# Kernel optimization log

Measured on AMD Instinct MI355X. Metric: run time of the kernel, lower is better.

## Reference

```python
import jax, jax.numpy as jnp
import numpy as np

LAYERS = 2
N_NODE = 100000
EMB = 112
BATCH = 512
SEQ = 50
NNZ = 1600000


def setup_inputs() -> dict:
    key = jax.random.key(0)
    ks = jax.random.split(key, 12)
    embedding = jax.random.normal(ks[0], (N_NODE, EMB), jnp.float32) * 0.1
    adj_rows = jax.random.randint(ks[1], (NNZ,), 0, N_NODE, jnp.int32)
    adj_cols = jax.random.randint(ks[2], (NNZ,), 0, N_NODE, jnp.int32)
    adj_vals = jax.random.uniform(ks[3], (NNZ,), jnp.float32) * 0.05  # normalized-ish weights
    W_q = jax.random.normal(ks[4], (EMB, EMB), jnp.float32) * 0.1
    W_k = jax.random.normal(ks[5], (EMB, EMB), jnp.float32) * 0.1
    w_sess = jax.random.normal(ks[6], (LAYERS, EMB, EMB), jnp.float32) * 0.1
    D = jax.random.uniform(ks[7], (BATCH, BATCH), jnp.float32) * 0.01
    A = jax.random.uniform(ks[8], (BATCH, BATCH), jnp.float32)
    session_len = jax.random.randint(ks[9], (BATCH, 1), 1, SEQ + 1, jnp.int32)
    mask = (jnp.arange(SEQ)[None, :] < session_len).astype(jnp.float32)  # [B,L]
    raw_items = jax.random.randint(ks[10], (BATCH, SEQ), 1, N_NODE + 1, jnp.int32)
    session_item = jnp.where(mask > 0, raw_items, 0)  # 0 = padding row in cl_embed
    return {
        "embedding": embedding, "adj_vals": adj_vals, "W_q": W_q, "W_k": W_k,
        "w_sess": w_sess, "D": D, "A": A, "adj_rows": adj_rows,
        "adj_cols": adj_cols, "session_item": session_item,
        "session_len": session_len, "mask": mask,
    }


def reference(embedding, adj_vals, W_q, W_k, w_sess, D, A,
              adj_rows, adj_cols, session_item, session_len, mask):
    dt = embedding.dtype
    # ---- HyperConv: layers x sparse.mm, then mean over layer stack ----
    emb = embedding
    acc = embedding
    for _ in range(LAYERS):
        msg = adj_vals[:, None] * emb[adj_cols]              # [nnz, d]
        emb = jax.ops.segment_sum(msg, adj_rows, num_segments=N_NODE)
        acc = acc + emb
    item_emb = acc / (LAYERS + 1)                            # [N, d]

    # ---- SR_IEM sigmoid attention pooling ----
    d = jnp.asarray(EMB, dt)
    cl = jnp.concatenate([jnp.zeros((1, EMB), dt), item_emb], axis=0)
    seq = cl[session_item]                                   # [B,L,d]
    Q = jax.nn.sigmoid(jnp.einsum('bld,de->ble', seq, W_q))
    K = jax.nn.sigmoid(jnp.einsum('bld,de->ble', seq, W_k))
    C = jax.nn.sigmoid(jnp.einsum('ble,bme->blm', Q, K)) / jnp.sqrt(d)  # [B,L,L]
    C = C * (mask[:, :, None] * mask[:, None, :])
    C = C * (1.0 - jnp.eye(SEQ, dtype=dt))                   # remove diagonal
    alpha = jnp.sum(C, axis=2) / session_len.astype(dt)      # [B,L]
    # per-session softmax over the first session_len positions == masked softmax
    beta = jax.nn.softmax(jnp.where(mask > 0, alpha, -1e9), axis=1)
    seq_h = jnp.einsum('bl,bld->bd', beta, seq)              # [B,d]

    # ---- SessConv propagation over session graph ----
    DA = D @ A                                               # [B,B]
    s = seq_h
    acc2 = seq_h
    for i in range(LAYERS):
        s = s @ w_sess[i].T                                  # Linear, no bias
        s = DA @ s
        norm = jnp.maximum(jnp.linalg.norm(s, axis=-1, keepdims=True), 1e-12)
        acc2 = acc2 + s / norm                               # F.normalize(p=2)
    return acc2 / (LAYERS + 1)                               # [B,d]
```

## Files before the change

### kernel.cpp

```cpp
#include <hip/hip_runtime.h>

#define N_NODE 100000
#define EMB 112
#define EMBP 128
#define BATCH 512
#define SEQL 50
#define NNZ 1600000
#define NROWS (BATCH * SEQL)

#define BROWS 256
#define NBUCK ((N_NODE + BROWS - 1) / BROWS)
#define BUCK_CAP 4608
#define TILE_E 6250
#define P1_BLOCKS 256

typedef _Float16 half2_t __attribute__((ext_vector_type(2)));

__device__ __forceinline__ float bf2f(unsigned short u) {
    return __uint_as_float((unsigned)u << 16);
}
__device__ __forceinline__ unsigned short f2bf(float f) {
    unsigned u = __float_as_uint(f);
    return (unsigned short)((u + 0x7FFF + ((u >> 16) & 1)) >> 16);
}
__device__ __forceinline__ float fdot2(half2_t a, half2_t b, float c) {
#if defined(__has_builtin)
#if __has_builtin(__builtin_amdgcn_fdot2)
    return __builtin_amdgcn_fdot2(a, b, c, false);
#else
    return c + (float)a[0] * (float)b[0] + (float)a[1] * (float)b[1];
#endif
#else
    return c + (float)a[0] * (float)b[0] + (float)a[1] * (float)b[1];
#endif
}

__global__ __launch_bounds__(256) void prep(
    const float* __restrict__ in, unsigned short* __restrict__ out)
{
    int i = blockIdx.x * 256 + threadIdx.x;
    int r = i >> 5, c = i & 31;
    ushort4 o; o.x = 0; o.y = 0; o.z = 0; o.w = 0;
    if (c < 28) {
        float4 v = ((const float4*)in)[r * 28 + c];
        o.x = f2bf(v.x); o.y = f2bf(v.y); o.z = f2bf(v.z); o.w = f2bf(v.w);
    }
    ((ushort4*)out)[i] = o;
}

__global__ __launch_bounds__(1024) void edge_bin(
    const int* __restrict__ rows, const int* __restrict__ cols,
    const float* __restrict__ vals,
    int* __restrict__ bcur, uint2* __restrict__ staged)
{
    __shared__ int hist[NBUCK];
    const int t = threadIdx.x;
    const int e0 = blockIdx.x * TILE_E;
    const int e1 = e0 + TILE_E;

    for (int i = t; i < NBUCK; i += 1024) hist[i] = 0;
    __syncthreads();
    for (int e = e0 + t; e < e1; e += 1024)
        atomicAdd(&hist[rows[e] >> 8], 1);
    __syncthreads();
    for (int i = t; i < NBUCK; i += 1024) {
        int c = hist[i];
        hist[i] = (c > 0) ? atomicAdd(&bcur[i], c) : 0;
    }
    __syncthreads();
    for (int e = e0 + t; e < e1; e += 1024) {
        int r = rows[e];
        int b = r >> 8;
        int k = atomicAdd(&hist[b], 1);
        uint2 s;
        s.x = ((unsigned)(r & 255) << 24) | (unsigned)cols[e];
        s.y = __float_as_uint(vals[e]);
        staged[(size_t)b * BUCK_CAP + k] = s;
    }
}

__global__ __launch_bounds__(1024) void bucket_csr_spmm(
    const uint2* __restrict__ staged, const int* __restrict__ bcur,
    const unsigned short* __restrict__ src, unsigned short* __restrict__ dst,
    int2* __restrict__ csr_cv, int* __restrict__ row_start,
    int* __restrict__ counts)
{
    __shared__ uint2 s_sorted[BUCK_CAP];
    __shared__ int cnt[BROWS];
    __shared__ int sc[BROWS];
    __shared__ int cur[BROWS];

    const int b = blockIdx.x;
    const int t = threadIdx.x;
    const int n = bcur[b];
    const size_t base = (size_t)b * BUCK_CAP;
    const int r0 = b << 8;

    if (t < BROWS) cnt[t] = 0;
    __syncthreads();
    for (int i = t; i < n; i += 1024)
        atomicAdd(&cnt[staged[base + i].x >> 24], 1);
    __syncthreads();

    if (t < BROWS) sc[t] = cnt[t];
    __syncthreads();
    for (int o = 1; o < BROWS; o <<= 1) {
        int v = 0;
        if (t < BROWS && t >= o) v = sc[t - o];
        __syncthreads();
        if (t < BROWS) sc[t] += v;
        __syncthreads();
    }
    if (t < BROWS) {
        int excl = sc[t] - cnt[t];
        cur[t] = excl;
        int row = r0 + t;
        if (row < N_NODE) {
            row_start[row] = (int)base + excl;
            counts[row] = cnt[t];
        }
    }
    __syncthreads();

    for (int i = t; i < n; i += 1024) {
        uint2 s = staged[base + i];
        int rl = s.x >> 24;
        int k = atomicAdd(&cur[rl], 1);
        uint2 e;
        e.x = s.x & 0x00FFFFFFu;
        e.y = s.y;
        s_sorted[k] = e;
    }
    __syncthreads();

    for (int i = t; i < n; i += 1024) {
        uint2 e = s_sorted[i];
        int2 cv; cv.x = (int)e.x; cv.y = (int)e.y;
        csr_cv[base + i] = cv;
    }

    const int wave = t >> 6;
    const int lane = t & 63;
    const int half = lane >> 5;
    const int hl = lane & 31;
    const int d0 = hl * 4;

    for (int it = 0; it < 8; ++it) {
        int rl = wave * 16 + it * 2 + half;
        int row = r0 + rl;
        bool valid = row < N_NODE;
        int n_r = valid ? cnt[rl] : 0;
        int beg = valid ? (sc[rl] - cnt[rl]) : 0;

        float a0 = 0.f, a1 = 0.f, a2 = 0.f, a3 = 0.f;
        int i = 0;
        for (; i + 8 <= n_r; i += 8) {
            #pragma unroll
            for (int j = 0; j < 8; ++j) {
                uint2 e = s_sorted[beg + i + j];
                float v = __uint_as_float(e.y);
                ushort4 u = *(const ushort4*)(src + (size_t)e.x * EMBP + d0);
                a0 += v * bf2f(u.x);
                a1 += v * bf2f(u.y);
                a2 += v * bf2f(u.z);
                a3 += v * bf2f(u.w);
            }
        }
        for (; i < n_r; ++i) {
            uint2 e = s_sorted[beg + i];
            float v = __uint_as_float(e.y);
            ushort4 u = *(const ushort4*)(src + (size_t)e.x * EMBP + d0);
            a0 += v * bf2f(u.x);
            a1 += v * bf2f(u.y);
            a2 += v * bf2f(u.z);
            a3 += v * bf2f(u.w);
        }
        if (valid) {
            ushort4 o;
            o.x = f2bf(a0); o.y = f2bf(a1); o.z = f2bf(a2); o.w = f2bf(a3);
            *(ushort4*)(dst + (size_t)row * EMBP + d0) = o;
        }
    }
}

__global__ __launch_bounds__(256) void gather_seq(
    const float* __restrict__ emb0,
    const unsigned short* __restrict__ e1b,
    const int2* __restrict__ csr_cv, const int* __restrict__ row_start,
    const int* __restrict__ counts,
    const int* __restrict__ items,
    float* __restrict__ seqg)
{
    const int t = threadIdx.x;
    const int hw = t >> 5;
    const int hl = t & 31;
    const int d0 = hl * 4;
    const int slot = blockIdx.x * 8 + hw;
    if (slot >= NROWS) return;

    float a0 = 0.f, a1 = 0.f, a2 = 0.f, a3 = 0.f;
    const int g = items[slot];
    if (g > 0) {
        const int r = g - 1;
        const int n = counts[r];
        const int beg = row_start[r];
        int i = 0;
        for (; i + 8 <= n; i += 8) {
            #pragma unroll
            for (int j = 0; j < 8; ++j) {
                int2 cv = csr_cv[beg + i + j];
                float v = __int_as_float(cv.y);
                ushort4 u = *(const ushort4*)(e1b + (size_t)cv.x * EMBP + d0);
                a0 += v * bf2f(u.x);
                a1 += v * bf2f(u.y);
                a2 += v * bf2f(u.z);
                a3 += v * bf2f(u.w);
            }
        }
        for (; i < n; ++i) {
            int2 cv = csr_cv[beg + i];
            float v = __int_as_float(cv.y);
            ushort4 u = *(const ushort4*)(e1b + (size_t)cv.x * EMBP + d0);
            a0 += v * bf2f(u.x);
            a1 += v * bf2f(u.y);
            a2 += v * bf2f(u.z);
            a3 += v * bf2f(u.w);
        }
        ushort4 u1 = *(const ushort4*)(e1b + (size_t)r * EMBP + d0);
        a0 += bf2f(u1.x); a1 += bf2f(u1.y); a2 += bf2f(u1.z); a3 += bf2f(u1.w);
        if (hl < 28) {
            float4 v0 = *(const float4*)(emb0 + (size_t)r * EMB + d0);
            a0 += v0.x; a1 += v0.y; a2 += v0.z; a3 += v0.w;
        }
        a0 *= (1.f / 3.f); a1 *= (1.f / 3.f);
        a2 *= (1.f / 3.f); a3 *= (1.f / 3.f);
    }
    if (hl < 28) {
        float4 w; w.x = a0; w.y = a1; w.z = a2; w.w = a3;
        *(float4*)(seqg + (size_t)slot * EMB + d0) = w;
    }
}

#define APAD 116
#define HPAD 120
struct AttnSmem {
    float s_seq[52][APAD];
    _Float16 sQ[SEQL][HPAD];
    _Float16 sK[SEQL][HPAD];
    float s_part[SEQL][4];
    float s_mask[SEQL];
    float s_beta[SEQL];
};
struct GemmSmem {
    float sD[32][33];
    float sA[32][33];
};
union AttnDaSmem { AttnSmem a; GemmSmem g; };

__global__ __launch_bounds__(256, 3) void attn_da(
    const float* __restrict__ seqg,
    const float* __restrict__ Wq, const float* __restrict__ Wk,
    const int* __restrict__ session_len, const float* __restrict__ mask,
    const float* __restrict__ D, const float* __restrict__ A,
    float* __restrict__ DA,
    float* __restrict__ seq_h, float* __restrict__ acc2)
{
    __shared__ AttnDaSmem sm;
    const int t = threadIdx.x;

    if (blockIdx.x >= BATCH) {
        const int bid = blockIdx.x - BATCH;
        const int i0 = (bid >> 4) * 32;
        const int j0 = (bid & 15) * 32;
        const int tx = t & 15;
        const int ty = t >> 4;
        float a00 = 0.f, a01 = 0.f, a10 = 0.f, a11 = 0.f;
        for (int k0 = 0; k0 < BATCH; k0 += 32) {
            for (int idx = t; idx < 1024; idx += 256) {
                int r = idx >> 5, c = idx & 31;
                sm.g.sD[r][c] = D[(i0 + r) * BATCH + k0 + c];
                sm.g.sA[r][c] = A[(k0 + r) * BATCH + j0 + c];
            }
            __syncthreads();
            #pragma unroll 8
            for (int kk = 0; kk < 32; ++kk) {
                float d0 = sm.g.sD[2 * ty][kk], d1 = sm.g.sD[2 * ty + 1][kk];
                float b0 = sm.g.sA[kk][2 * tx], b1 = sm.g.sA[kk][2 * tx + 1];
                a00 += d0 * b0; a01 += d0 * b1;
                a10 += d1 * b0; a11 += d1 * b1;
            }
            __syncthreads();
        }
        DA[(i0 + 2 * ty) * BATCH + j0 + 2 * tx] = a00;
        DA[(i0 + 2 * ty) * BATCH + j0 + 2 * tx + 1] = a01;
        DA[(i0 + 2 * ty + 1) * BATCH + j0 + 2 * tx] = a10;
        DA[(i0 + 2 * ty + 1) * BATCH + j0 + 2 * tx + 1] = a11;
        return;
    }

    const int b = blockIdx.x;

    for (int u = t; u < SEQL * 28; u += 256) {
        int l = u / 28;
        int q = u - l * 28;
        *(float4*)&sm.a.s_seq[l][q * 4] =
            *(const float4*)(seqg + (size_t)(b * SEQL + l) * EMB + q * 4);
    }
    if (t < 2 * 28) {
        int l = SEQL + (t / 28);
        int q = t - (t / 28) * 28;
        float4 z; z.x = 0.f; z.y = 0.f; z.z = 0.f; z.w = 0.f;
        *(float4*)&sm.a.s_seq[l][q * 4] = z;
    }
    if (t < SEQL) sm.a.s_mask[t] = mask[b * SEQL + t];
    __syncthreads();

    for (int u = t; u < 13 * 28; u += 256) {
        const int rg = u / 28;
        const int e0 = (u - rg * 28) * 4;
        float accq[4][4] = {{0.f}}, acck[4][4] = {{0.f}};
        #pragma unroll 2
        for (int d4 = 0; d4 < 28; ++d4) {
            float sa[4][4];
            #pragma unroll
            for (int rr = 0; rr < 4; ++rr) {
                float4 v = *(const float4*)&sm.a.s_seq[rg * 4 + rr][d4 * 4];
                sa[rr][0] = v.x; sa[rr][1] = v.y; sa[rr][2] = v.z; sa[rr][3] = v.w;
            }
            #pragma unroll
            for (int j = 0; j < 4; ++j) {
                const int d = d4 * 4 + j;
                float4 wq = *(const float4*)&Wq[d * EMB + e0];
                float4 wk = *(const float4*)&Wk[d * EMB + e0];
                #pragma unroll
                for (int rr = 0; rr < 4; ++rr) {
                    float s = sa[rr][j];
                    accq[rr][0] += s * wq.x; accq[rr][1] += s * wq.y;
                    accq[rr][2] += s * wq.z; accq[rr][3] += s * wq.w;
                    acck[rr][0] += s * wk.x; acck[rr][1] += s * wk.y;
                    acck[rr][2] += s * wk.z; acck[rr][3] += s * wk.w;
                }
            }
        }
        #pragma unroll
        for (int rr = 0; rr < 4; ++rr) {
            int row = rg * 4 + rr;
            if (row < SEQL) {
                float q0 = 1.f / (1.f + __expf(-accq[rr][0]));
                float q1 = 1.f / (1.f + __expf(-accq[rr][1]));
                float q2 = 1.f / (1.f + __expf(-accq[rr][2]));
                float q3 = 1.f / (1.f + __expf(-accq[rr][3]));
                float k0 = 1.f / (1.f + __expf(-acck[rr][0]));
                float k1 = 1.f / (1.f + __expf(-acck[rr][1]));
                float k2 = 1.f / (1.f + __expf(-acck[rr][2]));
                float k3 = 1.f / (1.f + __expf(-acck[rr][3]));
                half2_t hq0 = {(_Float16)q0, (_Float16)q1};
                half2_t hq1 = {(_Float16)q2, (_Float16)q3};
                half2_t hk0 = {(_Float16)k0, (_Float16)k1};
                half2_t hk1 = {(_Float16)k2, (_Float16)k3};
                *(half2_t*)&sm.a.sQ[row][e0]     = hq0;
                *(half2_t*)&sm.a.sQ[row][e0 + 2] = hq1;
                *(half2_t*)&sm.a.sK[row][e0]     = hk0;
                *(half2_t*)&sm.a.sK[row][e0 + 2] = hk1;
            }
        }
    }
    __syncthreads();

    const float inv_sqrt_d = rsqrtf((float)EMB);
    if (t < 200) {
        const int l = t >> 2;
        const int m0 = t & 3;
        float partial = 0.f;
        if (sm.a.s_mask[l] != 0.f) {
            const half2_t* qp = (const half2_t*)&sm.a.sQ[l][0];
            for (int m = m0; m < SEQL; m += 4) {
                if (m == l || sm.a.s_mask[m] == 0.f) continue;
                const half2_t* kp = (const half2_t*)&sm.a.sK[m][0];
                float d0 = 0.f, d1 = 0.f, d2 = 0.f, d3 = 0.f;
                #pragma unroll
                for (int d = 0; d < 56; d += 4) {
                    d0 = fdot2(qp[d],     kp[d],     d0);
                    d1 = fdot2(qp[d + 1], kp[d + 1], d1);
                    d2 = fdot2(qp[d + 2], kp[d + 2], d2);
                    d3 = fdot2(qp[d + 3], kp[d + 3], d3);
                }
                float dot = (d0 + d1) + (d2 + d3);
                partial += inv_sqrt_d / (1.f + __expf(-dot));
            }
        }
        sm.a.s_part[l][m0] = partial;
    }
    __syncthreads();

    if (t < 64) {
        float slen = (float)session_len[b];
        float a = -1e30f;
        if (t < SEQL && sm.a.s_mask[t] > 0.f)
            a = (sm.a.s_part[t][0] + sm.a.s_part[t][1] +
                 sm.a.s_part[t][2] + sm.a.s_part[t][3]) / slen;
        float mx = a;
        for (int o = 32; o > 0; o >>= 1) mx = fmaxf(mx, __shfl_xor(mx, o));
        float ex = __expf(a - mx);
        float sm_ = ex;
        for (int o = 32; o > 0; o >>= 1) sm_ += __shfl_xor(sm_, o);
        if (t < SEQL) sm.a.s_beta[t] = ex / sm_;
    }
    __syncthreads();

    if (t < EMB) {
        float h = 0.f;
        for (int l = 0; l < SEQL; ++l) h += sm.a.s_beta[l] * sm.a.s_seq[l][t];
        seq_h[b * EMB + t] = h;
        acc2[b * EMB + t] = h;
    }
}

__global__ __launch_bounds__(128) void sess_fused(
    const float* __restrict__ DA, const float* __restrict__ s_in,
    const float* __restrict__ W,
    float* __restrict__ s_out, float* __restrict__ acc2,
    float* __restrict__ out, int is_last)
{
    __shared__ float da[BATCH];
    __shared__ float u[EMB];
    __shared__ float red[128];
    const int b = blockIdx.x;
    const int e = threadIdx.x;

    for (int k = e; k < BATCH; k += 128) da[k] = DA[b * BATCH + k];
    __syncthreads();

    float uu = 0.f;
    if (e < EMB) {
        #pragma unroll 8
        for (int k = 0; k < BATCH; ++k) uu += da[k] * s_in[k * EMB + e];
        u[e] = uu;
    }
    __syncthreads();

    float v = 0.f;
    if (e < EMB) {
        #pragma unroll 8
        for (int d = 0; d < EMB; ++d) v += u[d] * W[e * EMB + d];
    }
    red[e] = (e < EMB) ? v * v : 0.f;
    __syncthreads();
    for (int off = 64; off > 0; off >>= 1) {
        if (e < off) red[e] += red[e + off];
        __syncthreads();
    }
    float nrm = fmaxf(sqrtf(red[0]), 1e-12f);
    if (e < EMB) {
        float a = acc2[b * EMB + e] + v / nrm;
        acc2[b * EMB + e] = a;
        s_out[b * EMB + e] = v;
        if (is_last) out[b * EMB + e] = a * (1.f / 3.f);
    }
}

extern "C" void kernel_launch(void* const* d_in, const int* in_sizes, int n_in,
                              void* d_out, int out_size, void* d_ws, size_t ws_size,
                              hipStream_t stream)
{
    (void)in_sizes; (void)n_in; (void)out_size; (void)ws_size;

    const float* embedding    = (const float*)d_in[0];
    const float* adj_vals     = (const float*)d_in[1];
    const float* W_q          = (const float*)d_in[2];
    const float* W_k          = (const float*)d_in[3];
    const float* w_sess       = (const float*)d_in[4];
    const float* D            = (const float*)d_in[5];
    const float* A            = (const float*)d_in[6];
    const int*   adj_rows     = (const int*)d_in[7];
    const int*   adj_cols     = (const int*)d_in[8];
    const int*   session_item = (const int*)d_in[9];
    const int*   session_len  = (const int*)d_in[10];
    const float* mask         = (const float*)d_in[11];
    float* out = (float*)d_out;

    unsigned short* ebf0 = (unsigned short*)d_ws;
    unsigned short* ebf1 = ebf0 + (size_t)N_NODE * EMBP;
    float* DAb       = (float*)(ebf1 + (size_t)N_NODE * EMBP);
    float* seqh      = DAb  + (size_t)BATCH * BATCH;
    float* acc2      = seqh + (size_t)BATCH * EMB;
    float* sbuf      = acc2 + (size_t)BATCH * EMB;
    int*   counts    = (int*)(sbuf + (size_t)BATCH * EMB);
    int*   row_start = counts + N_NODE;
    int*   bcur      = row_start + N_NODE;
    int2*  csr_cv    = (int2*)(bcur + 2048);
    uint2* staged    = (uint2*)(csr_cv + (size_t)NBUCK * BUCK_CAP);
    float* seqg      = (float*)staged;

    hipMemsetAsync(bcur, 0, 2048 * sizeof(int), stream);

    prep<<<N_NODE * 32 / 256, 256, 0, stream>>>(embedding, ebf0);

    edge_bin<<<P1_BLOCKS, 1024, 0, stream>>>(adj_rows, adj_cols, adj_vals,
                                             bcur, staged);

    bucket_csr_spmm<<<NBUCK, 1024, 0, stream>>>(staged, bcur, ebf0, ebf1,
                                                csr_cv, row_start, counts);

    gather_seq<<<NROWS / 8, 256, 0, stream>>>(embedding, ebf1, csr_cv,
                                              row_start, counts, session_item,
                                              seqg);

    attn_da<<<BATCH + 256, 256, 0, stream>>>(seqg, W_q, W_k, session_len, mask,
                                             D, A, DAb, seqh, acc2);

    sess_fused<<<BATCH, 128, 0, stream>>>(DAb, seqh, w_sess + 0 * EMB * EMB,
                                          sbuf, acc2, out, 0);
    sess_fused<<<BATCH, 128, 0, stream>>>(DAb, sbuf, w_sess + 1 * EMB * EMB,
                                          sbuf, acc2, out, 1);
}
```

Before: 330.1 us.

## Merge prep with edge binning and split CSR build from first SpMM layer

New measurement: 366.9 us. +11.1%, slower.

```diff
diff --git a/kernel.cpp b/kernel.cpp
--- a/kernel.cpp
+++ b/kernel.cpp
@@ -11,8 +11,10 @@
 #define BROWS 256
 #define NBUCK ((N_NODE + BROWS - 1) / BROWS)
 #define BUCK_CAP 4608
-#define TILE_E 6250
-#define P1_BLOCKS 256
+
+#define NPREP (N_NODE * 32 / 256)
+#define EB_BLOCKS 640
+#define EB_TILE 2500
 
 typedef _Float16 half2_t __attribute__((ext_vector_type(2)));
 
@@ -35,40 +37,42 @@
 #endif
 }
 
-__global__ __launch_bounds__(256) void prep(
-    const float* __restrict__ in, unsigned short* __restrict__ out)
-{
-    int i = blockIdx.x * 256 + threadIdx.x;
-    int r = i >> 5, c = i & 31;
-    ushort4 o; o.x = 0; o.y = 0; o.z = 0; o.w = 0;
-    if (c < 28) {
-        float4 v = ((const float4*)in)[r * 28 + c];
-        o.x = f2bf(v.x); o.y = f2bf(v.y); o.z = f2bf(v.z); o.w = f2bf(v.w);
-    }
-    ((ushort4*)out)[i] = o;
-}
-
-__global__ __launch_bounds__(1024) void edge_bin(
+__global__ __launch_bounds__(256) void prep_bin(
+    const float* __restrict__ in, unsigned short* __restrict__ out,
     const int* __restrict__ rows, const int* __restrict__ cols,
     const float* __restrict__ vals,
     int* __restrict__ bcur, uint2* __restrict__ staged)
 {
     __shared__ int hist[NBUCK];
     const int t = threadIdx.x;
-    const int e0 = blockIdx.x * TILE_E;
-    const int e1 = e0 + TILE_E;
-
-    for (int i = t; i < NBUCK; i += 1024) hist[i] = 0;
-    __syncthreads();
-    for (int e = e0 + t; e < e1; e += 1024)
+
+    if (blockIdx.x < NPREP) {
+        int i = blockIdx.x * 256 + t;
+        int r = i >> 5, c = i & 31;
+        ushort4 o; o.x = 0; o.y = 0; o.z = 0; o.w = 0;
+        if (c < 28) {
+            float4 v = ((const float4*)in)[r * 28 + c];
+            o.x = f2bf(v.x); o.y = f2bf(v.y); o.z = f2bf(v.z); o.w = f2bf(v.w);
+        }
+        ((ushort4*)out)[i] = o;
+        return;
+    }
+
+    const int eb = blockIdx.x - NPREP;
+    const int e0 = eb * EB_TILE;
+    const int e1 = e0 + EB_TILE;
+
+    for (int i = t; i < NBUCK; i += 256) hist[i] = 0;
+    __syncthreads();
+    for (int e = e0 + t; e < e1; e += 256)
         atomicAdd(&hist[rows[e] >> 8], 1);
     __syncthreads();
-    for (int i = t; i < NBUCK; i += 1024) {
+    for (int i = t; i < NBUCK; i += 256) {
         int c = hist[i];
         hist[i] = (c > 0) ? atomicAdd(&bcur[i], c) : 0;
     }
     __syncthreads();
-    for (int e = e0 + t; e < e1; e += 1024) {
+    for (int e = e0 + t; e < e1; e += 256) {
         int r = rows[e];
         int b = r >> 8;
         int k = atomicAdd(&hist[b], 1);
@@ -79,9 +83,8 @@
     }
 }
 
-__global__ __launch_bounds__(1024) void bucket_csr_spmm(
+__global__ __launch_bounds__(512) void bucket_csr(
     const uint2* __restrict__ staged, const int* __restrict__ bcur,
-    const unsigned short* __restrict__ src, unsigned short* __restrict__ dst,
     int2* __restrict__ csr_cv, int* __restrict__ row_start,
     int* __restrict__ counts)
 {
@@ -98,7 +101,7 @@
 
     if (t < BROWS) cnt[t] = 0;
     __syncthreads();
-    for (int i = t; i < n; i += 1024)
+    for (int i = t; i < n; i += 512)
         atomicAdd(&cnt[staged[base + i].x >> 24], 1);
     __syncthreads();
 
@@ -122,7 +125,7 @@
     }
     __syncthreads();
 
-    for (int i = t; i < n; i += 1024) {
+    for (int i = t; i < n; i += 512) {
         uint2 s = staged[base + i];
         int rl = s.x >> 24;
         int k = atomicAdd(&cur[rl], 1);
@@ -133,54 +136,54 @@
     }
     __syncthreads();
 
-    for (int i = t; i < n; i += 1024) {
+    for (int i = t; i < n; i += 512) {
         uint2 e = s_sorted[i];
         int2 cv; cv.x = (int)e.x; cv.y = (int)e.y;
         csr_cv[base + i] = cv;
     }
-
-    const int wave = t >> 6;
-    const int lane = t & 63;
-    const int half = lane >> 5;
-    const int hl = lane & 31;
+}
+
+__global__ __launch_bounds__(256) void spmm_l1(
+    const int2* __restrict__ csr_cv, const int* __restrict__ row_start,
+    const int* __restrict__ counts,
+    const unsigned short* __restrict__ src, unsigned short* __restrict__ dst)
+{
+    const int t = threadIdx.x;
+    const int hw = t >> 5;
+    const int hl = t & 31;
     const int d0 = hl * 4;
-
-    for (int it = 0; it < 8; ++it) {
-        int rl = wave * 16 + it * 2 + half;
-        int row = r0 + rl;
-        bool valid = row < N_NODE;
-        int n_r = valid ? cnt[rl] : 0;
-        int beg = valid ? (sc[rl] - cnt[rl]) : 0;
-
-        float a0 = 0.f, a1 = 0.f, a2 = 0.f, a3 = 0.f;
-        int i = 0;
-        for (; i + 8 <= n_r; i += 8) {
-            #pragma unroll
-            for (int j = 0; j < 8; ++j) {
-                uint2 e = s_sorted[beg + i + j];
-                float v = __uint_as_float(e.y);
-                ushort4 u = *(const ushort4*)(src + (size_t)e.x * EMBP + d0);
-                a0 += v * bf2f(u.x);
-                a1 += v * bf2f(u.y);
-                a2 += v * bf2f(u.z);
-                a3 += v * bf2f(u.w);
-            }
-        }
-        for (; i < n_r; ++i) {
-            uint2 e = s_sorted[beg + i];
-            float v = __uint_as_float(e.y);
-            ushort4 u = *(const ushort4*)(src + (size_t)e.x * EMBP + d0);
+    const int row = blockIdx.x * 8 + hw;
+    if (row >= N_NODE) return;
+
+    const int n = counts[row];
+    const int beg = row_start[row];
+
+    float a0 = 0.f, a1 = 0.f, a2 = 0.f, a3 = 0.f;
+    int i = 0;
+    for (; i + 8 <= n; i += 8) {
+        #pragma unroll
+        for (int j = 0; j < 8; ++j) {
+            int2 cv = csr_cv[beg + i + j];
+            float v = __int_as_float(cv.y);
+            ushort4 u = *(const ushort4*)(src + (size_t)cv.x * EMBP + d0);
             a0 += v * bf2f(u.x);
             a1 += v * bf2f(u.y);
             a2 += v * bf2f(u.z);
             a3 += v * bf2f(u.w);
         }
-        if (valid) {
-            ushort4 o;
-            o.x = f2bf(a0); o.y = f2bf(a1); o.z = f2bf(a2); o.w = f2bf(a3);
-            *(ushort4*)(dst + (size_t)row * EMBP + d0) = o;
-        }
-    }
+    }
+    for (; i < n; ++i) {
+        int2 cv = csr_cv[beg + i];
+        float v = __int_as_float(cv.y);
+        ushort4 u = *(const ushort4*)(src + (size_t)cv.x * EMBP + d0);
+        a0 += v * bf2f(u.x);
+        a1 += v * bf2f(u.y);
+        a2 += v * bf2f(u.z);
+        a3 += v * bf2f(u.w);
+    }
+    ushort4 o;
+    o.x = f2bf(a0); o.y = f2bf(a1); o.z = f2bf(a2); o.w = f2bf(a3);
+    *(ushort4*)(dst + (size_t)row * EMBP + d0) = o;
 }
 
 __global__ __launch_bounds__(256) void gather_seq(
@@ -494,13 +497,15 @@
 
     hipMemsetAsync(bcur, 0, 2048 * sizeof(int), stream);
 
-    prep<<<N_NODE * 32 / 256, 256, 0, stream>>>(embedding, ebf0);
-
-    edge_bin<<<P1_BLOCKS, 1024, 0, stream>>>(adj_rows, adj_cols, adj_vals,
-                                             bcur, staged);
-
-    bucket_csr_spmm<<<NBUCK, 1024, 0, stream>>>(staged, bcur, ebf0, ebf1,
-                                                csr_cv, row_start, counts);
+    prep_bin<<<NPREP + EB_BLOCKS, 256, 0, stream>>>(embedding, ebf0,
+                                                    adj_rows, adj_cols,
+                                                    adj_vals, bcur, staged);
+
+    bucket_csr<<<NBUCK, 512, 0, stream>>>(staged, bcur, csr_cv, row_start,
+                                          counts);
+
+    spmm_l1<<<(N_NODE + 7) / 8, 256, 0, stream>>>(csr_cv, row_start, counts,
+                                                  ebf0, ebf1);
 
     gather_seq<<<NROWS / 8, 256, 0, stream>>>(embedding, ebf1, csr_cv,
                                               row_start, counts, session_item,
```
